# Optimization experiments

Hardware: AMD Instinct MI355X
Metric: run time of the kernel (lower is better)

## Reference

```python
import jax, jax.numpy as jnp
import numpy as np

B, CIN, COUT, H, W = 64, 96, 96, 56, 56
MID = 192            # in_channels * expansion
SE_GROUPS = 12       # _nearest_divisor(192, 12)
SE_RED = 24          # ceil(max(192//8,4)/12)*12
EPS = 1e-5


def _apply_bn(x, p):
    # p: [4, C] = (gamma, beta, running_mean, running_var); eval-mode BN
    scale = p[0] * jax.lax.rsqrt(p[3] + EPS)
    shift = p[1] - p[2] * scale
    return x * scale[None, :, None, None] + shift[None, :, None, None]


def _shift_groups(x):
    h, w = x.shape[2], x.shape[3]
    x0, x1, x2, x3 = jnp.split(x, 4, axis=1)
    up = jnp.pad(x0, ((0, 0), (0, 0), (1, 0), (0, 0)))[:, :, :h, :]
    left = jnp.pad(x1, ((0, 0), (0, 0), (0, 0), (1, 0)))[:, :, :, :w]
    down = jnp.pad(x2, ((0, 0), (0, 0), (0, 1), (0, 0)))[:, :, 1:, :]
    right = jnp.pad(x3, ((0, 0), (0, 0), (0, 0), (0, 1)))[:, :, :, 1:]
    return jnp.concatenate([up, left, down, right], axis=1)


def _channel_shuffle(x, groups=4):
    b, c, h, w = x.shape
    x = x.reshape(b, groups, c // groups, h, w)
    x = jnp.transpose(x, (0, 2, 1, 3, 4))
    return x.reshape(b, c, h, w)


def _grouped_1x1(v, w, b, groups):
    # v: [B, Cin]; w: [Cout, Cin//groups, 1, 1]
    bsz = v.shape[0]
    cout = w.shape[0]
    vg = v.reshape(bsz, groups, -1)
    wg = w[:, :, 0, 0].reshape(groups, cout // groups, -1)
    out = jnp.einsum('bgi,goi->bgo', vg, wg).reshape(bsz, cout)
    return out + b


def _forward(x, expand_w, expand_bn, dw_w, dw_bn, id_w, id_bn, merge_bn,
             se_red_w, se_red_b, se_exp_w, se_exp_b, proj_w, proj_bn):
    # 1x1 expansion + BN + SiLU
    out = jnp.einsum('bchw,oc->bohw', x, expand_w[:, :, 0, 0])
    out = jax.nn.silu(_apply_bn(out, expand_bn))
    # shift-mix + channel shuffle (zero-FLOP data movement)
    out = _channel_shuffle(_shift_groups(out), groups=4)
    # depthwise 3x3 branch + BN
    dw = jax.lax.conv_general_dilated(
        out, dw_w, window_strides=(1, 1), padding=((1, 1), (1, 1)),
        feature_group_count=MID, dimension_numbers=('NCHW', 'OIHW', 'NCHW'))
    dw = _apply_bn(dw, dw_bn)
    # identity depthwise 1x1 branch (per-channel scale) + BN
    idb = _apply_bn(out * id_w[:, 0, 0, 0][None, :, None, None], id_bn)
    out = jax.nn.silu(_apply_bn(dw + idb, merge_bn))
    # grouped SE gating
    se = jnp.mean(out, axis=(2, 3))                     # [B, MID]
    se = jax.nn.relu(_grouped_1x1(se, se_red_w, se_red_b, SE_GROUPS))
    se = jax.nn.sigmoid(_grouped_1x1(se, se_exp_w, se_exp_b, SE_GROUPS))
    out = out * se[:, :, None, None]
    # 1x1 project + BN + residual + activation
    out = jnp.einsum('bchw,oc->bohw', out, proj_w[:, :, 0, 0])
    out = _apply_bn(out, proj_bn)
    out = out + x  # use_residual: stride==1 and in==out
    return jax.nn.silu(out)


def setup_inputs() -> dict:
    key = jax.random.key(0)
    ks = jax.random.split(key, 16)

    def bn_params(k, c):
        k1, k2, k3, k4 = jax.random.split(k, 4)
        gamma = 1.0 + 0.1 * jax.random.normal(k1, (c,), jnp.float32)
        beta = 0.1 * jax.random.normal(k2, (c,), jnp.float32)
        mean = 0.1 * jax.random.normal(k3, (c,), jnp.float32)
        var = 0.5 + jax.random.uniform(k4, (c,), jnp.float32)
        return jnp.stack([gamma, beta, mean, var])

    return {
        'x': jax.random.normal(ks[0], (B, CIN, H, W), jnp.float32),
        'expand_w': 0.1 * jax.random.normal(ks[1], (MID, CIN, 1, 1), jnp.float32),
        'expand_bn': bn_params(ks[2], MID),
        'dw_w': 0.2 * jax.random.normal(ks[3], (MID, 1, 3, 3), jnp.float32),
        'dw_bn': bn_params(ks[4], MID),
        'id_w': 0.2 * jax.random.normal(ks[5], (MID, 1, 1, 1), jnp.float32),
        'id_bn': bn_params(ks[6], MID),
        'merge_bn': bn_params(ks[7], MID),
        'se_red_w': 0.2 * jax.random.normal(ks[8], (SE_RED, MID // SE_GROUPS, 1, 1), jnp.float32),
        'se_red_b': 0.05 * jax.random.normal(ks[9], (SE_RED,), jnp.float32),
        'se_exp_w': 0.2 * jax.random.normal(ks[10], (MID, SE_RED // SE_GROUPS, 1, 1), jnp.float32),
        'se_exp_b': 0.05 * jax.random.normal(ks[11], (MID,), jnp.float32),
        'proj_w': 0.1 * jax.random.normal(ks[12], (COUT, MID, 1, 1), jnp.float32),
        'proj_bn': bn_params(ks[13], COUT),
    }


def reference(x, expand_w, expand_bn, dw_w, dw_bn, id_w, id_bn, merge_bn,
              se_red_w, se_red_b, se_exp_w, se_exp_b, proj_w, proj_bn):
    return _forward(x, expand_w, expand_bn, dw_w, dw_bn, id_w, id_bn, merge_bn,
                    se_red_w, se_red_b, se_exp_w, se_exp_b, proj_w, proj_bn)
```

## Files before the change

### kernel.cpp

```cpp
#include <hip/hip_runtime.h>
#include <hip/hip_bf16.h>

#define BB   64
#define CING 96
#define MIDC 192
#define HH   56
#define WWD  56
#define HWSZ (HH*WWD)
#define COUTC 96
#define BNEPS 1e-5f

typedef __attribute__((ext_vector_type(8))) short short8;
typedef __attribute__((ext_vector_type(8))) unsigned short ushort8v;
typedef __attribute__((ext_vector_type(4))) float float4v;
typedef unsigned short ushort_t;
typedef unsigned int uint_t;

__device__ __forceinline__ float siluf(float v){ return v / (1.f + __expf(-v)); }
__device__ __forceinline__ ushort_t f2bs(float f){
    uint_t u = __float_as_uint(f);
    uint_t r = u + 0x7FFFu + ((u >> 16) & 1u);
    return (ushort_t)(r >> 16);
}
__device__ __forceinline__ float bs2f(ushort_t u){
    return __uint_as_float(((uint_t)u) << 16);
}
__device__ __forceinline__ uint_t pkbf(float a, float b){
    __hip_bfloat162 h = __float22bfloat162_rn(make_float2(a, b));
    union { __hip_bfloat162 h; uint_t u; } cv; cv.h = h; return cv.u;
}
__device__ __forceinline__ float bslo(uint_t x){ return __uint_as_float(x << 16); }
__device__ __forceinline__ float bshi(uint_t x){ return __uint_as_float(x & 0xFFFF0000u); }

__global__ __launch_bounds__(256) void k0_setup(
    const float* __restrict__ expand_w, const float* __restrict__ expand_bn,
    const float* __restrict__ dw_w, const float* __restrict__ dw_bn,
    const float* __restrict__ id_w, const float* __restrict__ id_bn,
    const float* __restrict__ merge_bn,
    const float* __restrict__ proj_w, const float* __restrict__ proj_bn,
    ushort_t* __restrict__ Aexp, float* __restrict__ ebias,
    float* __restrict__ w9f, float* __restrict__ cstf,
    ushort_t* __restrict__ Aproj, float* __restrict__ pscf, float* __restrict__ pshf)
{
    int i = blockIdx.x*256 + threadIdx.x;
    if (i < 4608) {
        int m = i/24, kq = (i%24)*4;
        int ic = (m&3)*48 + (m>>2);
        float sc0 = expand_bn[ic]*rsqrtf(expand_bn[3*MIDC+ic]+BNEPS);
        #pragma unroll
        for (int j=0;j<4;j++) Aexp[m*96+kq+j] = f2bs(expand_w[ic*96+kq+j]*sc0);
        if (kq==0) ebias[m] = expand_bn[MIDC+ic] - expand_bn[2*MIDC+ic]*sc0;
    } else if (i < 9216) {
        int ii = i-4608; int m = ii/48, kq = (ii%48)*4;
        #pragma unroll
        for (int j=0;j<4;j++) Aproj[m*MIDC+kq+j] = f2bs(proj_w[m*MIDC+kq+j]);
        if (kq==0){
            float sc = proj_bn[m]*rsqrtf(proj_bn[3*COUTC+m]+BNEPS);
            pscf[m]=sc; pshf[m]=proj_bn[COUTC+m]-proj_bn[2*COUTC+m]*sc;
        }
    } else if (i < 9408) {
        int oc = i-9216;
        float sc1 = dw_bn[oc]    * rsqrtf(dw_bn[3*MIDC+oc]    + BNEPS);
        float sh1 = dw_bn[MIDC+oc]    - dw_bn[2*MIDC+oc]*sc1;
        float sc2 = id_bn[oc]    * rsqrtf(id_bn[3*MIDC+oc]    + BNEPS);
        float sh2 = id_bn[MIDC+oc]    - id_bn[2*MIDC+oc]*sc2;
        float sc3 = merge_bn[oc] * rsqrtf(merge_bn[3*MIDC+oc] + BNEPS);
        float sh3 = merge_bn[MIDC+oc] - merge_bn[2*MIDC+oc]*sc3;
        float A = sc3*sc1;
        #pragma unroll
        for (int j=0;j<9;j++) w9f[oc*9+j] = A*dw_w[oc*9+j];
        w9f[oc*9+4] += sc3*sc2*id_w[oc];
        cstf[oc] = sc3*(sh1+sh2) + sh3;
    }
}

#define LDB1T 104
__global__ __launch_bounds__(256) void k1_expand(
    const float* __restrict__ x,
    const ushort_t* __restrict__ Aexp,
    const float* __restrict__ ebias,
    ushort_t* __restrict__ EY)
{
    __shared__ __align__(16) ushort_t BsT[64*LDB1T];
    __shared__ float ebL[MIDC];
    const int t = threadIdx.x;
    const int p0 = blockIdx.x*64, b = blockIdx.y;

    if (t < MIDC) ebL[t] = ebias[t];
    {
        const int n  = t & 63;
        const int kb = (t >> 6)*24;
        #pragma unroll
        for (int ii = 0; ii < 3; ii++) {
            int k8 = kb + ii*8;
            const float* xp = x + ((size_t)(b*CING + k8))*HWSZ + p0 + n;
            ushort8v u;
            #pragma unroll
            for (int j = 0; j < 8; j++) u[j] = f2bs(xp[(size_t)j*HWSZ]);
            *(ushort8v*)(&BsT[n*LDB1T + k8]) = u;
        }
    }

    const int lane = t & 63, wv = t >> 6;
    const int l = lane & 15, q = lane >> 4;
    short8 af[3][3];
    #pragma unroll
    for (int ks = 0; ks < 3; ks++)
        #pragma unroll
        for (int mi = 0; mi < 3; mi++)
            af[ks][mi] = *(const short8*)(Aexp + ((wv*3+mi)*16 + l)*96 + ks*32 + q*8);
    __syncthreads();

    float4v acc[3][4];
    #pragma unroll
    for (int mi=0;mi<3;mi++)
        #pragma unroll
        for (int nt=0;nt<4;nt++) acc[mi][nt] = (float4v){0.f,0.f,0.f,0.f};
    #pragma unroll
    for (int ks = 0; ks < 3; ks++) {
        const int k0 = ks*32;
        short8 bf[4];
        #pragma unroll
        for (int nt = 0; nt < 4; nt++)
            bf[nt] = *(const short8*)(&BsT[(nt*16 + l)*LDB1T + k0 + q*8]);
        #pragma unroll
        for (int mi = 0; mi < 3; mi++)
            #pragma unroll
            for (int nt = 0; nt < 4; nt++)
                acc[mi][nt] = __builtin_amdgcn_mfma_f32_16x16x32_bf16(af[ks][mi], bf[nt], acc[mi][nt], 0,0,0);
    }
    #pragma unroll
    for (int mi = 0; mi < 3; mi++) {
        #pragma unroll
        for (int r = 0; r < 4; r++) {
            int m = (wv*3+mi)*16 + q*4 + r;
            float eb = ebL[m];
            size_t rowb = (size_t)(b*MIDC + m)*HWSZ + p0 + l;
            #pragma unroll
            for (int nt = 0; nt < 4; nt++)
                EY[rowb + nt*16] = f2bs(siluf(acc[mi][nt][r] + eb));
        }
    }
}

template<int DY, int DX>
__device__ __forceinline__ float dw_plane(
    ushort_t* __restrict__ plane, const float* __restrict__ w9, float cst,
    int li, int h, bool act)
{
    uint2 pA = make_uint2(0u,0u), pB = make_uint2(0u,0u);
    int rA = -100, rB = -100;
    if (h == 0) { if (DY==1){ rA=28; rB=29; } else if (DY==0){ rA=28; } }
    else        { if (DY==-1){ rA=26; rB=27; } else if (DY==0){ rA=27; } }
    const ushort_t* pl = plane + li*4;
    if (rA >= 0) pA = *(const uint2*)(pl + rA*WWD);
    if (rB >= 0) pB = *(const uint2*)(pl + rB*WWD);
    __syncthreads();

    const int ys = h ? 27 : -1;
    const int so = h ? 29 : 1;

    auto loadrow = [&](int y) -> uint2 {
        int yy = y + DY;
        uint2 u = make_uint2(0u,0u);
        if (((unsigned)y < (unsigned)HH) && ((unsigned)yy < (unsigned)HH)) {
            if (yy == rA)      u = pA;
            else if (yy == rB) u = pB;
            else               u = *(const uint2*)(pl + yy*WWD);
        }
        return u;
    };

    float p0[4] = {0,0,0,0}, p1[4] = {0,0,0,0};
    float partial = 0.f;
    uint2 u = loadrow(ys);
    for (int y = ys; y <= ys + 29; ++y) {
        uint2 un = loadrow(y + 1);
        uint_t lhi = __shfl_up(u.y, 1);
        uint_t rlo = __shfl_down(u.x, 1);
        if (li == 0)  lhi = 0u;
        if (li == 13) rlo = 0u;
        float s[8];
        s[0]=bslo(lhi); s[1]=bshi(lhi);
        s[2]=bslo(u.x); s[3]=bshi(u.x);
        s[4]=bslo(u.y); s[5]=bshi(u.y);
        s[6]=bslo(rlo); s[7]=bshi(rlo);
        if (li == 0)  s[DX+1] = 0.f;
        if (li == 13) s[DX+6] = 0.f;
        float o[4];
        #pragma unroll
        for (int j = 0; j < 4; j++) {
            float t0 = s[j+DX+1], t1 = s[j+DX+2], t2 = s[j+DX+3];
            o[j]  = p1[j] + (w9[6]*t0 + w9[7]*t1 + w9[8]*t2) + cst;
            p1[j] = p0[j] + (w9[3]*t0 + w9[4]*t1 + w9[5]*t2);
            p0[j] =          w9[0]*t0 + w9[1]*t1 + w9[2]*t2;
        }
        if (y >= so && act) {
            float y0=siluf(o[0]), y1=siluf(o[1]), y2=siluf(o[2]), y3=siluf(o[3]);
            uint2 w2; w2.x = pkbf(y0,y1); w2.y = pkbf(y2,y3);
            *(uint2*)(plane + (size_t)(y-1)*WWD + li*4) = w2;
            partial += (y0+y1) + (y2+y3);
        }
        u = un;
    }
    #pragma unroll
    for (int off = 1; off < 16; off <<= 1) partial += __shfl_xor(partial, off);
    return partial;
}

__global__ __launch_bounds__(128) void k2_dw(
    ushort_t* __restrict__ EY,
    const float* __restrict__ w9f,
    const float* __restrict__ cstf,
    float* __restrict__ sums)
{
    __shared__ float wred[8];
    const int t = threadIdx.x;
    const int lane = t & 63, h = t >> 6;
    const int lg = lane >> 4, li = lane & 15;
    const int gi = blockIdx.x >> 2, r = blockIdx.x & 3;
    const int b = blockIdx.y;
    const int oc = gi*16 + r + lg*4;
    ushort_t* plane = EY + (size_t)(b*MIDC + oc)*HWSZ;
    float w9[9];
    #pragma unroll
    for (int j = 0; j < 9; j++) w9[j] = w9f[oc*9+j];
    const float cst = cstf[oc];
    const bool act = (li < 14);
    float ps;
    if      (r == 0) ps = dw_plane<-1, 0>(plane, w9, cst, li, h, act);
    else if (r == 1) ps = dw_plane< 0,-1>(plane, w9, cst, li, h, act);
    else if (r == 2) ps = dw_plane< 1, 0>(plane, w9, cst, li, h, act);
    else             ps = dw_plane< 0, 1>(plane, w9, cst, li, h, act);
    if (li == 0) wred[h*4 + lg] = ps;
    __syncthreads();
    if (t < 4) sums[b*MIDC + gi*16 + r + t*4] = wred[t] + wred[4 + t];
}

__global__ __launch_bounds__(192) void k3_se(
    const float* __restrict__ sums,
    const float* __restrict__ se_red_w, const float* __restrict__ se_red_b,
    const float* __restrict__ se_exp_w, const float* __restrict__ se_exp_b,
    float* __restrict__ sews)
{
    __shared__ float meanL[MIDC];
    __shared__ float redL[24];
    const int b = blockIdx.x, t = threadIdx.x;
    meanL[t] = sums[b*MIDC + t] * (1.f/(float)HWSZ);
    __syncthreads();
    if (t < 24) {
        int g = t >> 1;
        float a = se_red_b[t];
        #pragma unroll
        for (int i = 0; i < 16; i++) a += meanL[g*16+i] * se_red_w[t*16+i];
        redL[t] = fmaxf(a, 0.f);
    }
    __syncthreads();
    int g = t >> 4;
    float a = se_exp_b[t] + redL[g*2]*se_exp_w[t*2] + redL[g*2+1]*se_exp_w[t*2+1];
    sews[b*MIDC + t] = 1.f/(1.f + __expf(-a));
}

#define LDB4T 200
__global__ __launch_bounds__(256) void k4_proj(
    const ushort_t* __restrict__ EY,
    const float* __restrict__ sews,
    const ushort_t* __restrict__ Aproj,
    const float* __restrict__ pscf, const float* __restrict__ pshf,
    const float* __restrict__ x,
    float* __restrict__ out)
{
    __shared__ __align__(16) ushort_t BsT[64*LDB4T];
    __shared__ float pscL[COUTC], pshL[COUTC];
    const int t = threadIdx.x;
    const int p0 = blockIdx.x*64, b = blockIdx.y;
    if (t < COUTC) { pscL[t] = pscf[t]; pshL[t] = pshf[t]; }
    {
        const int n  = t & 63;
        const int kb = (t >> 6)*48;
        const float* sew = sews + b*MIDC;
        #pragma unroll
        for (int ii = 0; ii < 6; ii++) {
            int k8 = kb + ii*8;
            const ushort_t* ep = EY + ((size_t)(b*MIDC + k8))*HWSZ + p0 + n;
            ushort8v u;
            #pragma unroll
            for (int j = 0; j < 8; j++)
                u[j] = f2bs(bs2f(ep[(size_t)j*HWSZ]) * sew[k8+j]);
            *(ushort8v*)(&BsT[n*LDB4T + k8]) = u;
        }
    }

    const int lane = t & 63, wv = t >> 6;
    const int l = lane & 15, q = lane >> 4;
    const int mh = wv >> 1, nh = wv & 1;
    short8 af[6][3];
    #pragma unroll
    for (int ks = 0; ks < 6; ks++)
        #pragma unroll
        for (int mi = 0; mi < 3; mi++)
            af[ks][mi] = *(const short8*)(Aproj + ((mh*3+mi)*16 + l)*MIDC + ks*32 + q*8);
    __syncthreads();

    float4v acc[3][2];
    #pragma unroll
    for (int mi=0;mi<3;mi++)
        #pragma unroll
        for (int nt=0;nt<2;nt++) acc[mi][nt] = (float4v){0.f,0.f,0.f,0.f};
    #pragma unroll
    for (int ks = 0; ks < 6; ks++) {
        const int k0 = ks*32;
        short8 bf[2];
        #pragma unroll
        for (int nt = 0; nt < 2; nt++)
            bf[nt] = *(const short8*)(&BsT[(nh*32 + nt*16 + l)*LDB4T + k0 + q*8]);
        #pragma unroll
        for (int mi = 0; mi < 3; mi++)
            #pragma unroll
            for (int nt = 0; nt < 2; nt++)
                acc[mi][nt] = __builtin_amdgcn_mfma_f32_16x16x32_bf16(af[ks][mi], bf[nt], acc[mi][nt], 0,0,0);
    }
    #pragma unroll
    for (int mi = 0; mi < 3; mi++) {
        #pragma unroll
        for (int r = 0; r < 4; r++) {
            int m = (mh*3+mi)*16 + q*4 + r;
            float sc = pscL[m], sh = pshL[m];
            size_t rowb = (size_t)(b*COUTC + m)*HWSZ + p0 + nh*32 + l;
            #pragma unroll
            for (int nt = 0; nt < 2; nt++) {
                size_t idx = rowb + nt*16;
                float v = acc[mi][nt][r]*sc + sh + x[idx];
                out[idx] = siluf(v);
            }
        }
    }
}

extern "C" void kernel_launch(void* const* d_in, const int* in_sizes, int n_in,
                              void* d_out, int out_size, void* d_ws, size_t ws_size,
                              hipStream_t stream)
{
    const float* x         = (const float*)d_in[0];
    const float* expand_w  = (const float*)d_in[1];
    const float* expand_bn = (const float*)d_in[2];
    const float* dw_w      = (const float*)d_in[3];
    const float* dw_bn     = (const float*)d_in[4];
    const float* id_w      = (const float*)d_in[5];
    const float* id_bn     = (const float*)d_in[6];
    const float* merge_bn  = (const float*)d_in[7];
    const float* se_red_w  = (const float*)d_in[8];
    const float* se_red_b  = (const float*)d_in[9];
    const float* se_exp_w  = (const float*)d_in[10];
    const float* se_exp_b  = (const float*)d_in[11];
    const float* proj_w    = (const float*)d_in[12];
    const float* proj_bn   = (const float*)d_in[13];

    char* base = (char*)d_ws;
    size_t off = 0;
    ushort_t* EY   = (ushort_t*)(base + off); off += (size_t)BB*MIDC*HWSZ*2;
    float* sums    = (float*)(base + off);    off += BB*MIDC*4;
    float* sews    = (float*)(base + off);    off += BB*MIDC*4;
    ushort_t* Aexp = (ushort_t*)(base + off); off += MIDC*CING*2;
    ushort_t* Aproj= (ushort_t*)(base + off); off += COUTC*MIDC*2;
    float* ebias   = (float*)(base + off);    off += MIDC*4;
    float* w9f     = (float*)(base + off);    off += MIDC*9*4;
    float* cstf    = (float*)(base + off);    off += MIDC*4;
    float* pscf    = (float*)(base + off);    off += COUTC*4;
    float* pshf    = (float*)(base + off);    off += COUTC*4;

    k0_setup<<<dim3(37), dim3(256), 0, stream>>>(
        expand_w, expand_bn, dw_w, dw_bn, id_w, id_bn, merge_bn, proj_w, proj_bn,
        Aexp, ebias, w9f, cstf, Aproj, pscf, pshf);
    k1_expand<<<dim3(HWSZ/64, BB), dim3(256), 0, stream>>>(x, Aexp, ebias, EY);
    k2_dw<<<dim3(48, BB), dim3(128), 0, stream>>>(EY, w9f, cstf, sums);
    k3_se<<<dim3(BB), dim3(192), 0, stream>>>(
        sums, se_red_w, se_red_b, se_exp_w, se_exp_b, sews);
    k4_proj<<<dim3(HWSZ/64, BB), dim3(256), 0, stream>>>(
        EY, sews, Aproj, pscf, pshf, x, (float*)d_out);
}
```

Baseline: 279.5 us.

## Fold setup and SE kernels into main kernels and stage epilogue stores via LDS

Removes the separate setup and SE kernels, so BN folding and weight bf16 conversion now run inside the expand, depthwise and projection kernels, and the SE MLP is recomputed per projection block. The expand and projection epilogues now write through shared memory and emit 16-byte coalesced global stores instead of scattered 2- and 4-byte stores. SiLU uses a hardware reciprocal, and the depthwise row loop is unrolled by two with loads issued ahead. This cuts two launches and improves store coalescing, at the cost of redundant per-block weight conversion and SE arithmetic plus extra barriers and LDS traffic.

```diff
diff --git a/kernel.cpp b/kernel.cpp
--- a/kernel.cpp
+++ b/kernel.cpp
@@ -16,7 +16,12 @@
 typedef unsigned short ushort_t;
 typedef unsigned int uint_t;
 
-__device__ __forceinline__ float siluf(float v){ return v / (1.f + __expf(-v)); }
+__device__ __forceinline__ float siluf(float v){
+    return v * __builtin_amdgcn_rcpf(1.f + __expf(-v));
+}
+__device__ __forceinline__ float sigmf(float v){
+    return __builtin_amdgcn_rcpf(1.f + __expf(-v));
+}
 __device__ __forceinline__ ushort_t f2bs(float f){
     uint_t u = __float_as_uint(f);
     uint_t r = u + 0x7FFFu + ((u >> 16) & 1u);
@@ -32,61 +37,27 @@
 __device__ __forceinline__ float bslo(uint_t x){ return __uint_as_float(x << 16); }
 __device__ __forceinline__ float bshi(uint_t x){ return __uint_as_float(x & 0xFFFF0000u); }
 
-__global__ __launch_bounds__(256) void k0_setup(
-    const float* __restrict__ expand_w, const float* __restrict__ expand_bn,
-    const float* __restrict__ dw_w, const float* __restrict__ dw_bn,
-    const float* __restrict__ id_w, const float* __restrict__ id_bn,
-    const float* __restrict__ merge_bn,
-    const float* __restrict__ proj_w, const float* __restrict__ proj_bn,
-    ushort_t* __restrict__ Aexp, float* __restrict__ ebias,
-    float* __restrict__ w9f, float* __restrict__ cstf,
-    ushort_t* __restrict__ Aproj, float* __restrict__ pscf, float* __restrict__ pshf)
-{
-    int i = blockIdx.x*256 + threadIdx.x;
-    if (i < 4608) {
-        int m = i/24, kq = (i%24)*4;
-        int ic = (m&3)*48 + (m>>2);
-        float sc0 = expand_bn[ic]*rsqrtf(expand_bn[3*MIDC+ic]+BNEPS);
-        #pragma unroll
-        for (int j=0;j<4;j++) Aexp[m*96+kq+j] = f2bs(expand_w[ic*96+kq+j]*sc0);
-        if (kq==0) ebias[m] = expand_bn[MIDC+ic] - expand_bn[2*MIDC+ic]*sc0;
-    } else if (i < 9216) {
-        int ii = i-4608; int m = ii/48, kq = (ii%48)*4;
-        #pragma unroll
-        for (int j=0;j<4;j++) Aproj[m*MIDC+kq+j] = f2bs(proj_w[m*MIDC+kq+j]);
-        if (kq==0){
-            float sc = proj_bn[m]*rsqrtf(proj_bn[3*COUTC+m]+BNEPS);
-            pscf[m]=sc; pshf[m]=proj_bn[COUTC+m]-proj_bn[2*COUTC+m]*sc;
-        }
-    } else if (i < 9408) {
-        int oc = i-9216;
-        float sc1 = dw_bn[oc]    * rsqrtf(dw_bn[3*MIDC+oc]    + BNEPS);
-        float sh1 = dw_bn[MIDC+oc]    - dw_bn[2*MIDC+oc]*sc1;
-        float sc2 = id_bn[oc]    * rsqrtf(id_bn[3*MIDC+oc]    + BNEPS);
-        float sh2 = id_bn[MIDC+oc]    - id_bn[2*MIDC+oc]*sc2;
-        float sc3 = merge_bn[oc] * rsqrtf(merge_bn[3*MIDC+oc] + BNEPS);
-        float sh3 = merge_bn[MIDC+oc] - merge_bn[2*MIDC+oc]*sc3;
-        float A = sc3*sc1;
-        #pragma unroll
-        for (int j=0;j<9;j++) w9f[oc*9+j] = A*dw_w[oc*9+j];
-        w9f[oc*9+4] += sc3*sc2*id_w[oc];
-        cstf[oc] = sc3*(sh1+sh2) + sh3;
-    }
-}
-
 #define LDB1T 104
+#define LDC1  72
 __global__ __launch_bounds__(256) void k1_expand(
     const float* __restrict__ x,
-    const ushort_t* __restrict__ Aexp,
-    const float* __restrict__ ebias,
+    const float* __restrict__ expand_w,
+    const float* __restrict__ expand_bn,
     ushort_t* __restrict__ EY)
 {
-    __shared__ __align__(16) ushort_t BsT[64*LDB1T];
-    __shared__ float ebL[MIDC];
+    __shared__ __align__(16) char smem[MIDC*LDC1*2];
+    __shared__ float scL[MIDC], ebL[MIDC];
+    ushort_t* BsT = (ushort_t*)smem;
+    ushort_t* Cs  = (ushort_t*)smem;
     const int t = threadIdx.x;
     const int p0 = blockIdx.x*64, b = blockIdx.y;
 
-    if (t < MIDC) ebL[t] = ebias[t];
+    if (t < MIDC) {
+        int ic = (t&3)*48 + (t>>2);
+        float sc = expand_bn[ic] * rsqrtf(expand_bn[3*MIDC+ic] + BNEPS);
+        scL[t] = sc;
+        ebL[t] = expand_bn[MIDC+ic] - expand_bn[2*MIDC+ic]*sc;
+    }
     {
         const int n  = t & 63;
         const int kb = (t >> 6)*24;
@@ -94,22 +65,35 @@
         for (int ii = 0; ii < 3; ii++) {
             int k8 = kb + ii*8;
             const float* xp = x + ((size_t)(b*CING + k8))*HWSZ + p0 + n;
-            ushort8v u;
-            #pragma unroll
-            for (int j = 0; j < 8; j++) u[j] = f2bs(xp[(size_t)j*HWSZ]);
-            *(ushort8v*)(&BsT[n*LDB1T + k8]) = u;
-        }
-    }
+            float v[8];
+            #pragma unroll
+            for (int j = 0; j < 8; j++) v[j] = xp[(size_t)j*HWSZ];
+            uint4 uu;
+            uu.x = pkbf(v[0],v[1]); uu.y = pkbf(v[2],v[3]);
+            uu.z = pkbf(v[4],v[5]); uu.w = pkbf(v[6],v[7]);
+            *(uint4*)(&BsT[n*LDB1T + k8]) = uu;
+        }
+    }
+    __syncthreads();
 
     const int lane = t & 63, wv = t >> 6;
     const int l = lane & 15, q = lane >> 4;
     short8 af[3][3];
     #pragma unroll
-    for (int ks = 0; ks < 3; ks++)
-        #pragma unroll
-        for (int mi = 0; mi < 3; mi++)
-            af[ks][mi] = *(const short8*)(Aexp + ((wv*3+mi)*16 + l)*96 + ks*32 + q*8);
-    __syncthreads();
+    for (int mi = 0; mi < 3; mi++) {
+        const int m = (wv*3+mi)*16 + l;
+        const float sc = scL[m];
+        const float* wp = expand_w + (size_t)((m&3)*48 + (m>>2))*CING + q*8;
+        #pragma unroll
+        for (int ks = 0; ks < 3; ks++) {
+            float4 v0 = *(const float4*)(wp + ks*32);
+            float4 v1 = *(const float4*)(wp + ks*32 + 4);
+            union { uint4 u; short8 s; } cv;
+            cv.u.x = pkbf(v0.x*sc, v0.y*sc); cv.u.y = pkbf(v0.z*sc, v0.w*sc);
+            cv.u.z = pkbf(v1.x*sc, v1.y*sc); cv.u.w = pkbf(v1.z*sc, v1.w*sc);
+            af[ks][mi] = cv.s;
+        }
+    }
 
     float4v acc[3][4];
     #pragma unroll
@@ -129,17 +113,25 @@
             for (int nt = 0; nt < 4; nt++)
                 acc[mi][nt] = __builtin_amdgcn_mfma_f32_16x16x32_bf16(af[ks][mi], bf[nt], acc[mi][nt], 0,0,0);
     }
+    __syncthreads();
     #pragma unroll
     for (int mi = 0; mi < 3; mi++) {
         #pragma unroll
         for (int r = 0; r < 4; r++) {
-            int m = (wv*3+mi)*16 + q*4 + r;
-            float eb = ebL[m];
-            size_t rowb = (size_t)(b*MIDC + m)*HWSZ + p0 + l;
+            const int m = (wv*3+mi)*16 + q*4 + r;
+            const float eb = ebL[m];
             #pragma unroll
             for (int nt = 0; nt < 4; nt++)
-                EY[rowb + nt*16] = f2bs(siluf(acc[mi][nt][r] + eb));
-        }
+                Cs[m*LDC1 + nt*16 + l] = f2bs(siluf(acc[mi][nt][r] + eb));
+        }
+    }
+    __syncthreads();
+    #pragma unroll
+    for (int i = 0; i < 6; i++) {
+        int ch = i*256 + t;
+        int row = ch >> 3, seg = ch & 7;
+        uint4 v = *(const uint4*)(&Cs[row*LDC1 + seg*8]);
+        *(uint4*)(EY + (size_t)(b*MIDC + row)*HWSZ + p0 + seg*8) = v;
     }
 }
 
@@ -171,11 +163,10 @@
         return u;
     };
 
-    float p0[4] = {0,0,0,0}, p1[4] = {0,0,0,0};
+    float p0v[4] = {0,0,0,0}, p1v[4] = {0,0,0,0};
     float partial = 0.f;
-    uint2 u = loadrow(ys);
-    for (int y = ys; y <= ys + 29; ++y) {
-        uint2 un = loadrow(y + 1);
+
+    auto process = [&](uint2 u, int y) {
         uint_t lhi = __shfl_up(u.y, 1);
         uint_t rlo = __shfl_down(u.x, 1);
         if (li == 0)  lhi = 0u;
@@ -191,9 +182,9 @@
         #pragma unroll
         for (int j = 0; j < 4; j++) {
             float t0 = s[j+DX+1], t1 = s[j+DX+2], t2 = s[j+DX+3];
-            o[j]  = p1[j] + (w9[6]*t0 + w9[7]*t1 + w9[8]*t2) + cst;
-            p1[j] = p0[j] + (w9[3]*t0 + w9[4]*t1 + w9[5]*t2);
-            p0[j] =          w9[0]*t0 + w9[1]*t1 + w9[2]*t2;
+            o[j]   = p1v[j] + (w9[6]*t0 + w9[7]*t1 + w9[8]*t2) + cst;
+            p1v[j] = p0v[j] + (w9[3]*t0 + w9[4]*t1 + w9[5]*t2);
+            p0v[j] =           w9[0]*t0 + w9[1]*t1 + w9[2]*t2;
         }
         if (y >= so && act) {
             float y0=siluf(o[0]), y1=siluf(o[1]), y2=siluf(o[2]), y3=siluf(o[3]);
@@ -201,7 +192,18 @@
             *(uint2*)(plane + (size_t)(y-1)*WWD + li*4) = w2;
             partial += (y0+y1) + (y2+y3);
         }
-        u = un;
+    };
+
+    uint2 u  = loadrow(ys);
+    uint2 un = loadrow(ys+1);
+    #pragma unroll
+    for (int k = 0; k < 15; k++) {
+        const int y = ys + 2*k;
+        uint2 u2 = loadrow(y+2);
+        uint2 u3 = loadrow(y+3);
+        process(u,  y);
+        process(un, y+1);
+        u = u2; un = u3;
     }
     #pragma unroll
     for (int off = 1; off < 16; off <<= 1) partial += __shfl_xor(partial, off);
@@ -210,8 +212,9 @@
 
 __global__ __launch_bounds__(128) void k2_dw(
     ushort_t* __restrict__ EY,
-    const float* __restrict__ w9f,
-    const float* __restrict__ cstf,
+    const float* __restrict__ dw_w,  const float* __restrict__ dw_bn,
+    const float* __restrict__ id_w,  const float* __restrict__ id_bn,
+    const float* __restrict__ merge_bn,
     float* __restrict__ sums)
 {
     __shared__ float wred[8];
@@ -222,10 +225,20 @@
     const int b = blockIdx.y;
     const int oc = gi*16 + r + lg*4;
     ushort_t* plane = EY + (size_t)(b*MIDC + oc)*HWSZ;
+
+    float sc1 = dw_bn[oc]    * rsqrtf(dw_bn[3*MIDC+oc]    + BNEPS);
+    float sh1 = dw_bn[MIDC+oc]    - dw_bn[2*MIDC+oc]*sc1;
+    float sc2 = id_bn[oc]    * rsqrtf(id_bn[3*MIDC+oc]    + BNEPS);
+    float sh2 = id_bn[MIDC+oc]    - id_bn[2*MIDC+oc]*sc2;
+    float sc3 = merge_bn[oc] * rsqrtf(merge_bn[3*MIDC+oc] + BNEPS);
+    float sh3 = merge_bn[MIDC+oc] - merge_bn[2*MIDC+oc]*sc3;
+    float A = sc3*sc1;
     float w9[9];
     #pragma unroll
-    for (int j = 0; j < 9; j++) w9[j] = w9f[oc*9+j];
-    const float cst = cstf[oc];
+    for (int j = 0; j < 9; j++) w9[j] = A*dw_w[oc*9+j];
+    w9[4] += sc3*sc2*id_w[oc];
+    const float cst = sc3*(sh1+sh2) + sh3;
+
     const bool act = (li < 14);
     float ps;
     if      (r == 0) ps = dw_plane<-1, 0>(plane, w9, cst, li, h, act);
@@ -237,16 +250,31 @@
     if (t < 4) sums[b*MIDC + gi*16 + r + t*4] = wred[t] + wred[4 + t];
 }
 
-__global__ __launch_bounds__(192) void k3_se(
+#define LDB4T 200
+#define LDC4  68
+__global__ __launch_bounds__(256) void k4_proj(
+    const ushort_t* __restrict__ EY,
     const float* __restrict__ sums,
     const float* __restrict__ se_red_w, const float* __restrict__ se_red_b,
     const float* __restrict__ se_exp_w, const float* __restrict__ se_exp_b,
-    float* __restrict__ sews)
+    const float* __restrict__ proj_w,   const float* __restrict__ proj_bn,
+    const float* __restrict__ x,
+    float* __restrict__ out)
 {
-    __shared__ float meanL[MIDC];
-    __shared__ float redL[24];
-    const int b = blockIdx.x, t = threadIdx.x;
-    meanL[t] = sums[b*MIDC + t] * (1.f/(float)HWSZ);
+    __shared__ __align__(16) char smem[COUTC*LDC4*4];
+    __shared__ float meanL[MIDC], redL[24], seL[MIDC];
+    __shared__ float pscL[COUTC], pshL[COUTC];
+    ushort_t* BsT = (ushort_t*)smem;
+    float*    Cs4 = (float*)smem;
+    const int t = threadIdx.x;
+    const int p0 = blockIdx.x*64, b = blockIdx.y;
+
+    if (t < MIDC) meanL[t] = sums[b*MIDC + t] * (1.f/(float)HWSZ);
+    if (t < COUTC) {
+        float sc = proj_bn[t] * rsqrtf(proj_bn[3*COUTC+t] + BNEPS);
+        pscL[t] = sc;
+        pshL[t] = proj_bn[COUTC+t] - proj_bn[2*COUTC+t]*sc;
+    }
     __syncthreads();
     if (t < 24) {
         int g = t >> 1;
@@ -256,38 +284,28 @@
         redL[t] = fmaxf(a, 0.f);
     }
     __syncthreads();
-    int g = t >> 4;
-    float a = se_exp_b[t] + redL[g*2]*se_exp_w[t*2] + redL[g*2+1]*se_exp_w[t*2+1];
-    sews[b*MIDC + t] = 1.f/(1.f + __expf(-a));
-}
-
-#define LDB4T 200
-__global__ __launch_bounds__(256) void k4_proj(
-    const ushort_t* __restrict__ EY,
-    const float* __restrict__ sews,
-    const ushort_t* __restrict__ Aproj,
-    const float* __restrict__ pscf, const float* __restrict__ pshf,
-    const float* __restrict__ x,
-    float* __restrict__ out)
-{
-    __shared__ __align__(16) ushort_t BsT[64*LDB4T];
-    __shared__ float pscL[COUTC], pshL[COUTC];
-    const int t = threadIdx.x;
-    const int p0 = blockIdx.x*64, b = blockIdx.y;
-    if (t < COUTC) { pscL[t] = pscf[t]; pshL[t] = pshf[t]; }
+    if (t < MIDC) {
+        int g = t >> 4;
+        float a = se_exp_b[t] + redL[g*2]*se_exp_w[t*2] + redL[g*2+1]*se_exp_w[t*2+1];
+        seL[t] = sigmf(a);
+    }
+    __syncthreads();
+
     {
         const int n  = t & 63;
         const int kb = (t >> 6)*48;
-        const float* sew = sews + b*MIDC;
         #pragma unroll
         for (int ii = 0; ii < 6; ii++) {
             int k8 = kb + ii*8;
             const ushort_t* ep = EY + ((size_t)(b*MIDC + k8))*HWSZ + p0 + n;
-            ushort8v u;
+            float v[8];
             #pragma unroll
             for (int j = 0; j < 8; j++)
-                u[j] = f2bs(bs2f(ep[(size_t)j*HWSZ]) * sew[k8+j]);
-            *(ushort8v*)(&BsT[n*LDB4T + k8]) = u;
+                v[j] = bs2f(ep[(size_t)j*HWSZ]) * seL[k8+j];
+            uint4 uu;
+            uu.x = pkbf(v[0],v[1]); uu.y = pkbf(v[2],v[3]);
+            uu.z = pkbf(v[4],v[5]); uu.w = pkbf(v[6],v[7]);
+            *(uint4*)(&BsT[n*LDB4T + k8]) = uu;
         }
     }
 
@@ -296,10 +314,19 @@
     const int mh = wv >> 1, nh = wv & 1;
     short8 af[6][3];
     #pragma unroll
-    for (int ks = 0; ks < 6; ks++)
-        #pragma unroll
-        for (int mi = 0; mi < 3; mi++)
-            af[ks][mi] = *(const short8*)(Aproj + ((mh*3+mi)*16 + l)*MIDC + ks*32 + q*8);
+    for (int mi = 0; mi < 3; mi++) {
+        const int m = (mh*3+mi)*16 + l;
+        const float* wp = proj_w + (size_t)m*MIDC + q*8;
+        #pragma unroll
+        for (int ks = 0; ks < 6; ks++) {
+            float4 v0 = *(const float4*)(wp + ks*32);
+            float4 v1 = *(const float4*)(wp + ks*32 + 4);
+            union { uint4 u; short8 s; } cv;
+            cv.u.x = pkbf(v0.x, v0.y); cv.u.y = pkbf(v0.z, v0.w);
+            cv.u.z = pkbf(v1.x, v1.y); cv.u.w = pkbf(v1.z, v1.w);
+            af[ks][mi] = cv.s;
+        }
+    }
     __syncthreads();
 
     float4v acc[3][2];
@@ -320,20 +347,30 @@
             for (int nt = 0; nt < 2; nt++)
                 acc[mi][nt] = __builtin_amdgcn_mfma_f32_16x16x32_bf16(af[ks][mi], bf[nt], acc[mi][nt], 0,0,0);
     }
+    __syncthreads();
     #pragma unroll
     for (int mi = 0; mi < 3; mi++) {
         #pragma unroll
         for (int r = 0; r < 4; r++) {
-            int m = (mh*3+mi)*16 + q*4 + r;
-            float sc = pscL[m], sh = pshL[m];
-            size_t rowb = (size_t)(b*COUTC + m)*HWSZ + p0 + nh*32 + l;
-            #pragma unroll
-            for (int nt = 0; nt < 2; nt++) {
-                size_t idx = rowb + nt*16;
-                float v = acc[mi][nt][r]*sc + sh + x[idx];
-                out[idx] = siluf(v);
-            }
-        }
+            const int m = (mh*3+mi)*16 + q*4 + r;
+            const float sc = pscL[m], sh = pshL[m];
+            #pragma unroll
+            for (int nt = 0; nt < 2; nt++)
+                Cs4[m*LDC4 + nh*32 + nt*16 + l] = acc[mi][nt][r]*sc + sh;
+        }
+    }
+    __syncthreads();
+    #pragma unroll
+    for (int i = 0; i < 6; i++) {
+        int ch = i*256 + t;
+        int row = ch >> 4, seg = ch & 15;
+        const size_t idx = (size_t)(b*COUTC + row)*HWSZ + p0 + seg*4;
+        float4 c = *(const float4*)(&Cs4[row*LDC4 + seg*4]);
+        float4 xr = *(const float4*)(x + idx);
+        float4 o;
+        o.x = siluf(c.x + xr.x); o.y = siluf(c.y + xr.y);
+        o.z = siluf(c.z + xr.z); o.w = siluf(c.w + xr.w);
+        *(float4*)(out + idx) = o;
     }
 }
 
@@ -357,25 +394,14 @@
     const float* proj_bn   = (const float*)d_in[13];
 
     char* base = (char*)d_ws;
-    size_t off = 0;
-    ushort_t* EY   = (ushort_t*)(base + off); off += (size_t)BB*MIDC*HWSZ*2;
-    float* sums    = (float*)(base + off);    off += BB*MIDC*4;
-    float* sews    = (float*)(base + off);    off += BB*MIDC*4;
-    ushort_t* Aexp = (ushort_t*)(base + off); off += MIDC*CING*2;
-    ushort_t* Aproj= (ushort_t*)(base + off); off += COUTC*MIDC*2;
-    float* ebias   = (float*)(base + off);    off += MIDC*4;
-    float* w9f     = (float*)(base + off);    off += MIDC*9*4;
-    float* cstf    = (float*)(base + off);    off += MIDC*4;
-    float* pscf    = (float*)(base + off);    off += COUTC*4;
-    float* pshf    = (float*)(base + off);    off += COUTC*4;
-
-    k0_setup<<<dim3(37), dim3(256), 0, stream>>>(
-        expand_w, expand_bn, dw_w, dw_bn, id_w, id_bn, merge_bn, proj_w, proj_bn,
-        Aexp, ebias, w9f, cstf, Aproj, pscf, pshf);
-    k1_expand<<<dim3(HWSZ/64, BB), dim3(256), 0, stream>>>(x, Aexp, ebias, EY);
-    k2_dw<<<dim3(48, BB), dim3(128), 0, stream>>>(EY, w9f, cstf, sums);
-    k3_se<<<dim3(BB), dim3(192), 0, stream>>>(
-        sums, se_red_w, se_red_b, se_exp_w, se_exp_b, sews);
+    ushort_t* EY = (ushort_t*)base;
+    float* sums  = (float*)(base + (size_t)BB*MIDC*HWSZ*2);
+
+    k1_expand<<<dim3(HWSZ/64, BB), dim3(256), 0, stream>>>(
+        x, expand_w, expand_bn, EY);
+    k2_dw<<<dim3(48, BB), dim3(128), 0, stream>>>(
+        EY, dw_w, dw_bn, id_w, id_bn, merge_bn, sums);
     k4_proj<<<dim3(HWSZ/64, BB), dim3(256), 0, stream>>>(
-        EY, sews, Aproj, pscf, pshf, x, (float*)d_out);
-}
+        EY, sums, se_red_w, se_red_b, se_exp_w, se_exp_b,
+        proj_w, proj_bn, x, (float*)d_out);
+}
```

New measurement: 322.7 us. 1.15x slower.
